# Optimization experiments

Hardware: AMD Instinct MI355X
Metric: run time of the kernel (lower is better)

The kernel has to match this reference:

```python
import jax, jax.numpy as jnp
import numpy as np

N = 100000       # nodes
E = 1600000      # edges (avg degree 16)
C_IN = 128
C_OUT = 64
C_HID = 2 * C_OUT  # 128, matches GCNEncoder's 2*out_channels hidden width


def setup_inputs() -> dict:
    key = jax.random.key(0)
    k1, k2, k3, k4 = jax.random.split(key, 4)
    x = jax.random.normal(k1, (N, C_IN), dtype=jnp.float32)
    edge_index = jax.random.randint(k2, (2, E), 0, N, dtype=jnp.int64)
    # Glorot-ish scale for the linear weights (PyG GCNConv uses glorot init)
    W1 = jax.random.normal(k3, (C_IN, C_HID), dtype=jnp.float32) / np.sqrt(C_IN)
    b1 = jnp.zeros((C_HID,), dtype=jnp.float32)
    W2 = jax.random.normal(k4, (C_HID, C_OUT), dtype=jnp.float32) / np.sqrt(C_HID)
    b2 = jnp.zeros((C_OUT,), dtype=jnp.float32)
    return {"x": x, "edge_index": edge_index, "W1": W1, "b1": b1, "W2": W2, "b2": b2}


def _gcn_conv(x, src, dst, norm_e, self_norm, W, b):
    # GCNConv: out = D^{-1/2} (A + I) D^{-1/2} (x @ W) + b
    h = x @ W                                   # [N, C'] transform first (cheaper)
    msg = h[src] * norm_e[:, None]              # [E, C'] gather + edge normalization
    agg = jax.ops.segment_sum(msg, dst, num_segments=N)  # scatter-add over targets
    return agg + self_norm[:, None] * h + b     # self-loop term + bias


def reference(x, edge_index, W1, b1, W2, b2):
    src, dst = edge_index[0], edge_index[1]
    # degrees on A + I (self-loops added), identical for both layers
    deg = jax.ops.segment_sum(jnp.ones((E,), jnp.float32), dst, num_segments=N) + 1.0
    dinv = jax.lax.rsqrt(deg)                   # deg >= 1, no zero-guard needed
    norm_e = dinv[src] * dinv[dst]              # [E]
    self_norm = dinv * dinv                     # [N]

    h = _gcn_conv(x, src, dst, norm_e, self_norm, W1, b1)
    h = jax.nn.relu(h)
    return _gcn_conv(h, src, dst, norm_e, self_norm, W2, b2)
```

## Files before the change

kernel.cpp:

```cpp
#include <hip/hip_runtime.h>
#include <hip/hip_fp16.h>

#define NN   100000
#define NE   1600000
#define CIN  128
#define CHID 128
#define COUT 64

#define NPB  256
#define NB   391
#define NBLK 128
#define CHUNK ((NE + NBLK - 1) / NBLK)
#define BPAD 2048

typedef _Float16 f16x8 __attribute__((ext_vector_type(8)));
typedef float    f32x4 __attribute__((ext_vector_type(4)));

#define NTILE 782
#define GGRID 512

__global__ void k_zrow(__half* __restrict__ g1, __half* __restrict__ g2) {
  int t = threadIdx.x;
  if (t < 128) g1[(size_t)NN * CHID + t] = __float2half(0.f);
  if (t < 64)  g2[(size_t)NN * COUT + t] = __float2half(0.f);
}

__global__ __launch_bounds__(512) void k_passA(const int* __restrict__ dst,
                                               int* __restrict__ tab) {
  __shared__ int hist[NB];
  int tid = threadIdx.x;
  for (int t = tid; t < NB; t += 512) hist[t] = 0;
  __syncthreads();
  int i0 = blockIdx.x * CHUNK;
  int i1 = min(i0 + CHUNK, NE);
  for (int i = i0 + tid; i < i1; i += 512)
    atomicAdd(&hist[((unsigned)dst[i]) >> 8], 1);
  __syncthreads();
  for (int t = tid; t < NB; t += 512)
    tab[t * NBLK + blockIdx.x] = hist[t];
}

__global__ __launch_bounds__(512) void k_bscan(const int* __restrict__ tab,
                                               int* __restrict__ bb) {
  __shared__ int s[512];
  int t = threadIdx.x;
  int v = 0;
  if (t < NB) {
    const int* row = tab + t * NBLK;
#pragma unroll 8
    for (int k = 0; k < NBLK; k++) v += row[k];
  }
  s[t] = v;
  __syncthreads();
  for (int off = 1; off < 512; off <<= 1) {
    int u = (t >= off) ? s[t - off] : 0;
    __syncthreads();
    s[t] += u;
    __syncthreads();
  }
  if (t < NB) bb[t] = s[t] - v;
  if (t == 0) bb[NB] = NE;
}

__global__ __launch_bounds__(128) void k_tabscan(int* __restrict__ tab,
                                                 const int* __restrict__ bb) {
  __shared__ int s[128];
  int b = blockIdx.x, t = threadIdx.x;
  int v = tab[b * NBLK + t];
  s[t] = v;
  __syncthreads();
  for (int off = 1; off < 128; off <<= 1) {
    int u = (t >= off) ? s[t - off] : 0;
    __syncthreads();
    s[t] += u;
    __syncthreads();
  }
  tab[b * NBLK + t] = bb[b] + s[t] - v;
}

__global__ __launch_bounds__(512) void k_passB(const int* __restrict__ src,
                                               const int* __restrict__ dst,
                                               const int* __restrict__ tab,
                                               int* __restrict__ barr) {
  __shared__ int cur[NB];
  int tid = threadIdx.x;
  for (int t = tid; t < NB; t += 512) cur[t] = tab[t * NBLK + blockIdx.x];
  __syncthreads();
  int i0 = blockIdx.x * CHUNK;
  int i1 = min(i0 + CHUNK, NE);
  for (int i = i0 + tid; i < i1; i += 512) {
    int d = dst[i];
    unsigned b = ((unsigned)d) >> 8;
    int p = atomicAdd(&cur[b], 1);
    barr[p] = (src[i] << 8) | (d & 255);
  }
}

__global__ __launch_bounds__(256) void k_l2(const int* __restrict__ barr,
                                            const int* __restrict__ bb,
                                            int* __restrict__ csr,
                                            int* __restrict__ rs,
                                            int* __restrict__ re,
                                            float* __restrict__ dinv) {
  __shared__ int lcnt[NPB];
  __shared__ int lcur[NPB];
  int b = blockIdx.x, t = threadIdx.x;
  int e0 = bb[b], e1 = bb[b + 1];
  lcnt[t] = 0;
  __syncthreads();
  for (int i = e0 + t; i < e1; i += 256) atomicAdd(&lcnt[barr[i] & 255], 1);
  __syncthreads();
  int v = lcnt[t];
  int pv = (v + 7) & ~7;
  lcur[t] = pv;
  __syncthreads();
  for (int off = 1; off < 256; off <<= 1) {
    int u = (t >= off) ? lcur[t - off] : 0;
    __syncthreads();
    lcur[t] += u;
    __syncthreads();
  }
  int pex = lcur[t] - pv;
  int start = e0 + b * BPAD + pex;
  int g = b * NPB + t;
  if (g < NN) {
    rs[g] = start;
    re[g] = start + pv;
    dinv[g] = rsqrtf((float)v + 1.0f);
  }
  __syncthreads();
  lcur[t] = start;
  for (int k = v; k < pv; k++) csr[start + k] = NN;
  __syncthreads();
  for (int i = e0 + t; i < e1; i += 256) {
    int w = barr[i];
    int p = atomicAdd(&lcur[w & 255], 1);
    csr[p] = ((unsigned)w) >> 8;
  }
}

__global__ __launch_bounds__(256, 2) void k_gemm1(const float* __restrict__ X,
                                                  const float* __restrict__ W,
                                                  const float* __restrict__ dinv,
                                                  __half* __restrict__ G) {
  __shared__ _Float16 Wt[128][128];
  int tid = threadIdx.x;
  for (int i = tid; i < 128 * 32; i += 256) {
    int k = i >> 5, c4 = (i & 31) << 2;
    float4 v = ((const float4*)W)[i];
    Wt[c4 + 0][k] = (_Float16)v.x;
    Wt[c4 + 1][k] = (_Float16)v.y;
    Wt[c4 + 2][k] = (_Float16)v.z;
    Wt[c4 + 3][k] = (_Float16)v.w;
  }
  __syncthreads();
  int wv = tid >> 6, lane = tid & 63;
  int l15 = lane & 15, g = lane >> 4;

  f16x8 wf[8][4];
#pragma unroll
  for (int cf = 0; cf < 8; cf++)
#pragma unroll
    for (int ks = 0; ks < 4; ks++)
      wf[cf][ks] = *(const f16x8*)&Wt[cf * 16 + l15][ks * 32 + g * 8];

  for (int t = blockIdx.x; t < NTILE; t += GGRID) {
    int rowbase = t * 128 + wv * 32;
    f32x4 acc[2][8];
#pragma unroll
    for (int i = 0; i < 2; i++)
#pragma unroll
      for (int j = 0; j < 8; j++) acc[i][j] = (f32x4){0.f, 0.f, 0.f, 0.f};

    int r0 = min(rowbase + l15, NN - 1);
    int r1 = min(rowbase + 16 + l15, NN - 1);
    const float* p0 = X + (size_t)r0 * CIN + g * 8;
    const float* p1 = X + (size_t)r1 * CIN + g * 8;

    float4 u0a = *(const float4*)p0, u0b = *(const float4*)(p0 + 4);
    float4 u1a = *(const float4*)p1, u1b = *(const float4*)(p1 + 4);

#pragma unroll
    for (int ks = 0; ks < 4; ks++) {
      f16x8 xa, xb;
      xa[0] = (_Float16)u0a.x; xa[1] = (_Float16)u0a.y;
      xa[2] = (_Float16)u0a.z; xa[3] = (_Float16)u0a.w;
      xa[4] = (_Float16)u0b.x; xa[5] = (_Float16)u0b.y;
      xa[6] = (_Float16)u0b.z; xa[7] = (_Float16)u0b.w;
      xb[0] = (_Float16)u1a.x; xb[1] = (_Float16)u1a.y;
      xb[2] = (_Float16)u1a.z; xb[3] = (_Float16)u1a.w;
      xb[4] = (_Float16)u1b.x; xb[5] = (_Float16)u1b.y;
      xb[6] = (_Float16)u1b.z; xb[7] = (_Float16)u1b.w;
      if (ks < 3) {
        int o = (ks + 1) * 32;
        u0a = *(const float4*)(p0 + o); u0b = *(const float4*)(p0 + o + 4);
        u1a = *(const float4*)(p1 + o); u1b = *(const float4*)(p1 + o + 4);
      }
#pragma unroll
      for (int cf = 0; cf < 8; cf++) {
        acc[0][cf] = __builtin_amdgcn_mfma_f32_16x16x32_f16(wf[cf][ks], xa, acc[0][cf], 0, 0, 0);
        acc[1][cf] = __builtin_amdgcn_mfma_f32_16x16x32_f16(wf[cf][ks], xb, acc[1][cf], 0, 0, 0);
      }
    }

#pragma unroll
    for (int rf = 0; rf < 2; rf++) {
      int row = rowbase + rf * 16 + l15;
      if (row < NN) {
        float dn = dinv[row];
#pragma unroll
        for (int cf = 0; cf < 8; cf++) {
          int col = cf * 16 + g * 4;
          __half2 h0 = __half2(__float2half(dn * acc[rf][cf][0]),
                               __float2half(dn * acc[rf][cf][1]));
          __half2 h1 = __half2(__float2half(dn * acc[rf][cf][2]),
                               __float2half(dn * acc[rf][cf][3]));
          uint2 s;
          s.x = *(unsigned*)&h0;
          s.y = *(unsigned*)&h1;
          *(uint2*)(G + (size_t)row * CHID + col) = s;
        }
      }
    }
  }
}

__global__ __launch_bounds__(256, 2) void k_gemm2(const __half* __restrict__ X,
                                                  const float* __restrict__ W,
                                                  const float* __restrict__ dinv,
                                                  __half* __restrict__ G) {
  __shared__ _Float16 Wt[64][128];
  int tid = threadIdx.x;
  for (int i = tid; i < 128 * 16; i += 256) {
    int k = i >> 4, c4 = (i & 15) << 2;
    float4 v = ((const float4*)W)[i];
    Wt[c4 + 0][k] = (_Float16)v.x;
    Wt[c4 + 1][k] = (_Float16)v.y;
    Wt[c4 + 2][k] = (_Float16)v.z;
    Wt[c4 + 3][k] = (_Float16)v.w;
  }
  __syncthreads();
  int wv = tid >> 6, lane = tid & 63;
  int l15 = lane & 15, g = lane >> 4;

  f16x8 wf[4][4];
#pragma unroll
  for (int cf = 0; cf < 4; cf++)
#pragma unroll
    for (int ks = 0; ks < 4; ks++)
      wf[cf][ks] = *(const f16x8*)&Wt[cf * 16 + l15][ks * 32 + g * 8];

  for (int t = blockIdx.x; t < NTILE; t += GGRID) {
    int rowbase = t * 128 + wv * 32;
    f32x4 acc[2][4];
#pragma unroll
    for (int i = 0; i < 2; i++)
#pragma unroll
      for (int j = 0; j < 4; j++) acc[i][j] = (f32x4){0.f, 0.f, 0.f, 0.f};

    int r0 = min(rowbase + l15, NN - 1);
    int r1 = min(rowbase + 16 + l15, NN - 1);
    const _Float16* p0 = (const _Float16*)X + (size_t)r0 * CHID + g * 8;
    const _Float16* p1 = (const _Float16*)X + (size_t)r1 * CHID + g * 8;

    f16x8 xa = *(const f16x8*)p0;
    f16x8 xb = *(const f16x8*)p1;

#pragma unroll
    for (int ks = 0; ks < 4; ks++) {
      f16x8 ca = xa, cb = xb;
      if (ks < 3) {
        int o = (ks + 1) * 32;
        xa = *(const f16x8*)(p0 + o);
        xb = *(const f16x8*)(p1 + o);
      }
#pragma unroll
      for (int cf = 0; cf < 4; cf++) {
        acc[0][cf] = __builtin_amdgcn_mfma_f32_16x16x32_f16(wf[cf][ks], ca, acc[0][cf], 0, 0, 0);
        acc[1][cf] = __builtin_amdgcn_mfma_f32_16x16x32_f16(wf[cf][ks], cb, acc[1][cf], 0, 0, 0);
      }
    }

#pragma unroll
    for (int rf = 0; rf < 2; rf++) {
      int row = rowbase + rf * 16 + l15;
      if (row < NN) {
        float dn = dinv[row];
#pragma unroll
        for (int cf = 0; cf < 4; cf++) {
          int col = cf * 16 + g * 4;
          __half2 h0 = __half2(__float2half(dn * acc[rf][cf][0]),
                               __float2half(dn * acc[rf][cf][1]));
          __half2 h1 = __half2(__float2half(dn * acc[rf][cf][2]),
                               __float2half(dn * acc[rf][cf][3]));
          uint2 s;
          s.x = *(unsigned*)&h0;
          s.y = *(unsigned*)&h1;
          *(uint2*)(G + (size_t)row * COUT + col) = s;
        }
      }
    }
  }
}

#define ACC8(A, V)                                                  \
  {                                                                 \
    float2 f;                                                       \
    f = __half22float2(*(__half2*)&(V).x); A[0] += f.x; A[1] += f.y; \
    f = __half22float2(*(__half2*)&(V).y); A[2] += f.x; A[3] += f.y; \
    f = __half22float2(*(__half2*)&(V).z); A[4] += f.x; A[5] += f.y; \
    f = __half22float2(*(__half2*)&(V).w); A[6] += f.x; A[7] += f.y; \
  }

__global__ __launch_bounds__(256) void k_agg1(const __half* __restrict__ g,
                                              const int* __restrict__ rs,
                                              const int* __restrict__ re,
                                              const float* __restrict__ dinv,
                                              const int* __restrict__ csr,
                                              const float* __restrict__ b,
                                              __half* __restrict__ o) {
  int wid = (blockIdx.x * blockDim.x + threadIdx.x) >> 6;
  int lane = threadIdx.x & 63;
  if (wid >= NN) return;
  int q = lane >> 4, ql = lane & 15;
  const uint4* gp = (const uint4*)g;

  float aA[8] = {0.f, 0.f, 0.f, 0.f, 0.f, 0.f, 0.f, 0.f};
  float aB[8] = {0.f, 0.f, 0.f, 0.f, 0.f, 0.f, 0.f, 0.f};

  if (q == 0) {
    uint4 v = gp[(size_t)wid * 16 + ql];
    ACC8(aA, v);
  }

  int i0 = rs[wid], i1 = re[wid];
  for (int i = i0; i < i1; i += 8) {
    int sA = csr[i + q];
    int sB = csr[i + 4 + q];
    uint4 vA = gp[(size_t)sA * 16 + ql];
    uint4 vB = gp[(size_t)sB * 16 + ql];
    ACC8(aA, vA);
    ACC8(aB, vB);
  }

  float r[8];
#pragma unroll
  for (int c = 0; c < 8; c++) {
    float t = aA[c] + aB[c];
    t += __shfl_xor(t, 16);
    t += __shfl_xor(t, 32);
    r[c] = t;
  }
  if (q == 0) {
    float dn = dinv[wid];
    float4 b0 = *(const float4*)(b + 8 * ql);
    float4 b1 = *(const float4*)(b + 8 * ql + 4);
    __half2 h[4];
    h[0] = __half2(__float2half(fmaxf(fmaf(dn, r[0], b0.x), 0.f)),
                   __float2half(fmaxf(fmaf(dn, r[1], b0.y), 0.f)));
    h[1] = __half2(__float2half(fmaxf(fmaf(dn, r[2], b0.z), 0.f)),
                   __float2half(fmaxf(fmaf(dn, r[3], b0.w), 0.f)));
    h[2] = __half2(__float2half(fmaxf(fmaf(dn, r[4], b1.x), 0.f)),
                   __float2half(fmaxf(fmaf(dn, r[5], b1.y), 0.f)));
    h[3] = __half2(__float2half(fmaxf(fmaf(dn, r[6], b1.z), 0.f)),
                   __float2half(fmaxf(fmaf(dn, r[7], b1.w), 0.f)));
    *(uint4*)(o + (size_t)wid * CHID + 8 * ql) = *(uint4*)h;
  }
}

__global__ __launch_bounds__(256) void k_agg2(const __half* __restrict__ g,
                                              const int* __restrict__ rs,
                                              const int* __restrict__ re,
                                              const float* __restrict__ dinv,
                                              const int* __restrict__ csr,
                                              const float* __restrict__ b,
                                              float* __restrict__ o) {
  int wid = (blockIdx.x * blockDim.x + threadIdx.x) >> 6;
  int lane = threadIdx.x & 63;
  if (wid >= NN) return;
  int g8 = lane >> 3, gl = lane & 7;
  const uint4* gp = (const uint4*)g;

  float aA[8] = {0.f, 0.f, 0.f, 0.f, 0.f, 0.f, 0.f, 0.f};

  if (g8 == 0) {
    uint4 v = gp[(size_t)wid * 8 + gl];
    ACC8(aA, v);
  }

  int i0 = rs[wid], i1 = re[wid];
  for (int i = i0; i < i1; i += 8) {
    int s = csr[i + g8];
    uint4 v = gp[(size_t)s * 8 + gl];
    ACC8(aA, v);
  }

  float r[8];
#pragma unroll
  for (int c = 0; c < 8; c++) {
    float t = aA[c];
    t += __shfl_xor(t, 8);
    t += __shfl_xor(t, 16);
    t += __shfl_xor(t, 32);
    r[c] = t;
  }
  if (g8 == 0) {
    float dn = dinv[wid];
    float4 b0 = *(const float4*)(b + 8 * gl);
    float4 b1 = *(const float4*)(b + 8 * gl + 4);
    float4 o0 = make_float4(fmaf(dn, r[0], b0.x), fmaf(dn, r[1], b0.y),
                            fmaf(dn, r[2], b0.z), fmaf(dn, r[3], b0.w));
    float4 o1v = make_float4(fmaf(dn, r[4], b1.x), fmaf(dn, r[5], b1.y),
                             fmaf(dn, r[6], b1.z), fmaf(dn, r[7], b1.w));
    *(float4*)(o + (size_t)wid * COUT + 8 * gl) = o0;
    *(float4*)(o + (size_t)wid * COUT + 8 * gl + 4) = o1v;
  }
}


extern "C" void kernel_launch(void* const* d_in, const int* in_sizes, int n_in,
                              void* d_out, int out_size, void* d_ws, size_t ws_size,
                              hipStream_t stream) {
  const float* x  = (const float*)d_in[0];
  const int*   ei = (const int*)d_in[1];
  const float* W1 = (const float*)d_in[2];
  const float* b1 = (const float*)d_in[3];
  const float* W2 = (const float*)d_in[4];
  const float* b2 = (const float*)d_in[5];
  float* out = (float*)d_out;

  const int* esrc = ei;
  const int* edst = ei + NE;

  char* p = (char*)d_ws;
  __half* g1 = (__half*)p;    p += (size_t)(NN + 1) * CHID * 2;
  __half* o1 = (__half*)p;    p += (size_t)NN * CHID * 2;
  __half* g2 = (__half*)p;    p += (size_t)(NN + 1) * COUT * 2;
  int* rs  = (int*)p;         p += (size_t)NN * 4;
  int* re  = (int*)p;         p += (size_t)NN * 4;
  float* dinv = (float*)p;    p += (size_t)NN * 4;
  int* tab = (int*)p;         p += (size_t)NB * NBLK * 4;
  int* bb  = (int*)p;         p += (size_t)(NB + 1) * 4;
  int* barr = (int*)p;        p += (size_t)NE * 4;
  int* csr = (int*)p;         p += (size_t)(NE + NB * BPAD) * 4;

  hipLaunchKernelGGL(k_zrow, dim3(1), dim3(128), 0, stream, g1, g2);

  hipLaunchKernelGGL(k_passA, dim3(NBLK), dim3(512), 0, stream, edst, tab);
  hipLaunchKernelGGL(k_bscan, dim3(1), dim3(512), 0, stream, tab, bb);
  hipLaunchKernelGGL(k_tabscan, dim3(NB), dim3(128), 0, stream, tab, bb);
  hipLaunchKernelGGL(k_passB, dim3(NBLK), dim3(512), 0, stream, esrc, edst, tab, barr);
  hipLaunchKernelGGL(k_l2, dim3(NB), dim3(256), 0, stream, barr, bb, csr, rs, re, dinv);

  hipLaunchKernelGGL(k_gemm1, dim3(GGRID), dim3(256), 0, stream, x, W1, dinv, g1);
  hipLaunchKernelGGL(k_agg1, dim3((NN + 3) / 4), dim3(256), 0, stream, g1, rs, re, dinv, csr, b1, o1);

  hipLaunchKernelGGL(k_gemm2, dim3(GGRID), dim3(256), 0, stream, o1, W2, dinv, g2);
  hipLaunchKernelGGL(k_agg2, dim3((NN + 3) / 4), dim3(256), 0, stream, g2, rs, re, dinv, csr, b2, out);
}
```

Before: 224.3 us.

## Merge scan kernels, fold zero-row init into k_l2, unroll aggregation gathers

Merges the block-base scan and per-table scan into a single one-block kernel that walks each table row serially with int4 accesses. Moves the zero-padding-row initialization into k_l2 so one kernel launch disappears. Unrolls the neighbor-gather loops in both aggregation kernels to 16 edges per iteration with extra accumulators, so more independent loads are in flight per wave. Risks: the serial row scan in one block may be slower than the previous 391-block parallel scan, and the extra accumulators raise register pressure.

Measured after the change: 227.1 us. Within noise of the previous version (+1.3%).

```diff
diff --git a/kernel.cpp b/kernel.cpp
--- a/kernel.cpp
+++ b/kernel.cpp
@@ -19,12 +19,6 @@
 #define NTILE 782
 #define GGRID 512
 
-__global__ void k_zrow(__half* __restrict__ g1, __half* __restrict__ g2) {
-  int t = threadIdx.x;
-  if (t < 128) g1[(size_t)NN * CHID + t] = __float2half(0.f);
-  if (t < 64)  g2[(size_t)NN * COUT + t] = __float2half(0.f);
-}
-
 __global__ __launch_bounds__(512) void k_passA(const int* __restrict__ dst,
                                                int* __restrict__ tab) {
   __shared__ int hist[NB];
@@ -40,8 +34,8 @@
     tab[t * NBLK + blockIdx.x] = hist[t];
 }
 
-__global__ __launch_bounds__(512) void k_bscan(const int* __restrict__ tab,
-                                               int* __restrict__ bb) {
+__global__ __launch_bounds__(512) void k_scan(int* __restrict__ tab,
+                                              int* __restrict__ bb) {
   __shared__ int s[512];
   int t = threadIdx.x;
   int v = 0;
@@ -58,24 +52,22 @@
     s[t] += u;
     __syncthreads();
   }
-  if (t < NB) bb[t] = s[t] - v;
+  int base = s[t] - v;
+  if (t < NB) bb[t] = base;
   if (t == 0) bb[NB] = NE;
-}
-
-__global__ __launch_bounds__(128) void k_tabscan(int* __restrict__ tab,
-                                                 const int* __restrict__ bb) {
-  __shared__ int s[128];
-  int b = blockIdx.x, t = threadIdx.x;
-  int v = tab[b * NBLK + t];
-  s[t] = v;
-  __syncthreads();
-  for (int off = 1; off < 128; off <<= 1) {
-    int u = (t >= off) ? s[t - off] : 0;
-    __syncthreads();
-    s[t] += u;
-    __syncthreads();
-  }
-  tab[b * NBLK + t] = bb[b] + s[t] - v;
+  if (t < NB) {
+    int run = base;
+    int* row = tab + t * NBLK;
+    for (int k = 0; k < NBLK; k += 4) {
+      int4 c = *(int4*)(row + k);
+      int4 w;
+      w.x = run; run += c.x;
+      w.y = run; run += c.y;
+      w.z = run; run += c.z;
+      w.w = run; run += c.w;
+      *(int4*)(row + k) = w;
+    }
+  }
 }
 
 __global__ __launch_bounds__(512) void k_passB(const int* __restrict__ src,
@@ -101,10 +93,16 @@
                                             int* __restrict__ csr,
                                             int* __restrict__ rs,
                                             int* __restrict__ re,
-                                            float* __restrict__ dinv) {
+                                            float* __restrict__ dinv,
+                                            __half* __restrict__ g1,
+                                            __half* __restrict__ g2) {
   __shared__ int lcnt[NPB];
   __shared__ int lcur[NPB];
   int b = blockIdx.x, t = threadIdx.x;
+  if (b == 0) {
+    if (t < 128) g1[(size_t)NN * CHID + t] = __float2half(0.f);
+    if (t < 64)  g2[(size_t)NN * COUT + t] = __float2half(0.f);
+  }
   int e0 = bb[b], e1 = bb[b + 1];
   lcnt[t] = 0;
   __syncthreads();
@@ -327,6 +325,8 @@
 
   float aA[8] = {0.f, 0.f, 0.f, 0.f, 0.f, 0.f, 0.f, 0.f};
   float aB[8] = {0.f, 0.f, 0.f, 0.f, 0.f, 0.f, 0.f, 0.f};
+  float aC[8] = {0.f, 0.f, 0.f, 0.f, 0.f, 0.f, 0.f, 0.f};
+  float aD[8] = {0.f, 0.f, 0.f, 0.f, 0.f, 0.f, 0.f, 0.f};
 
   if (q == 0) {
     uint4 v = gp[(size_t)wid * 16 + ql];
@@ -334,19 +334,30 @@
   }
 
   int i0 = rs[wid], i1 = re[wid];
-  for (int i = i0; i < i1; i += 8) {
+  int i = i0;
+  for (; i + 16 <= i1; i += 16) {
+    int sA = csr[i + q];
+    int sB = csr[i + 4 + q];
+    int sC = csr[i + 8 + q];
+    int sD = csr[i + 12 + q];
+    uint4 vA = gp[(size_t)sA * 16 + ql];
+    uint4 vB = gp[(size_t)sB * 16 + ql];
+    uint4 vC = gp[(size_t)sC * 16 + ql];
+    uint4 vD = gp[(size_t)sD * 16 + ql];
+    ACC8(aA, vA); ACC8(aB, vB); ACC8(aC, vC); ACC8(aD, vD);
+  }
+  if (i < i1) {
     int sA = csr[i + q];
     int sB = csr[i + 4 + q];
     uint4 vA = gp[(size_t)sA * 16 + ql];
     uint4 vB = gp[(size_t)sB * 16 + ql];
-    ACC8(aA, vA);
-    ACC8(aB, vB);
+    ACC8(aA, vA); ACC8(aB, vB);
   }
 
   float r[8];
 #pragma unroll
   for (int c = 0; c < 8; c++) {
-    float t = aA[c] + aB[c];
+    float t = (aA[c] + aB[c]) + (aC[c] + aD[c]);
     t += __shfl_xor(t, 16);
     t += __shfl_xor(t, 32);
     r[c] = t;
@@ -382,6 +393,7 @@
   const uint4* gp = (const uint4*)g;
 
   float aA[8] = {0.f, 0.f, 0.f, 0.f, 0.f, 0.f, 0.f, 0.f};
+  float aB[8] = {0.f, 0.f, 0.f, 0.f, 0.f, 0.f, 0.f, 0.f};
 
   if (g8 == 0) {
     uint4 v = gp[(size_t)wid * 8 + gl];
@@ -389,7 +401,15 @@
   }
 
   int i0 = rs[wid], i1 = re[wid];
-  for (int i = i0; i < i1; i += 8) {
+  int i = i0;
+  for (; i + 16 <= i1; i += 16) {
+    int sA = csr[i + g8];
+    int sB = csr[i + 8 + g8];
+    uint4 vA = gp[(size_t)sA * 8 + gl];
+    uint4 vB = gp[(size_t)sB * 8 + gl];
+    ACC8(aA, vA); ACC8(aB, vB);
+  }
+  if (i < i1) {
     int s = csr[i + g8];
     uint4 v = gp[(size_t)s * 8 + gl];
     ACC8(aA, v);
@@ -398,7 +418,7 @@
   float r[8];
 #pragma unroll
   for (int c = 0; c < 8; c++) {
-    float t = aA[c];
+    float t = aA[c] + aB[c];
     t += __shfl_xor(t, 8);
     t += __shfl_xor(t, 16);
     t += __shfl_xor(t, 32);
@@ -444,17 +464,17 @@
   int* barr = (int*)p;        p += (size_t)NE * 4;
   int* csr = (int*)p;         p += (size_t)(NE + NB * BPAD) * 4;
 
-  hipLaunchKernelGGL(k_zrow, dim3(1), dim3(128), 0, stream, g1, g2);
-
   hipLaunchKernelGGL(k_passA, dim3(NBLK), dim3(512), 0, stream, edst, tab);
-  hipLaunchKernelGGL(k_bscan, dim3(1), dim3(512), 0, stream, tab, bb);
-  hipLaunchKernelGGL(k_tabscan, dim3(NB), dim3(128), 0, stream, tab, bb);
+  hipLaunchKernelGGL(k_scan, dim3(1), dim3(512), 0, stream, tab, bb);
   hipLaunchKernelGGL(k_passB, dim3(NBLK), dim3(512), 0, stream, esrc, edst, tab, barr);
-  hipLaunchKernelGGL(k_l2, dim3(NB), dim3(256), 0, stream, barr, bb, csr, rs, re, dinv);
+  hipLaunchKernelGGL(k_l2, dim3(NB), dim3(256), 0, stream, barr, bb, csr, rs, re,
+                     dinv, g1, g2);
 
   hipLaunchKernelGGL(k_gemm1, dim3(GGRID), dim3(256), 0, stream, x, W1, dinv, g1);
-  hipLaunchKernelGGL(k_agg1, dim3((NN + 3) / 4), dim3(256), 0, stream, g1, rs, re, dinv, csr, b1, o1);
+  hipLaunchKernelGGL(k_agg1, dim3((NN + 3) / 4), dim3(256), 0, stream,
+                     g1, rs, re, dinv, csr, b1, o1);
 
   hipLaunchKernelGGL(k_gemm2, dim3(GGRID), dim3(256), 0, stream, o1, W2, dinv, g2);
-  hipLaunchKernelGGL(k_agg2, dim3((NN + 3) / 4), dim3(256), 0, stream, g2, rs, re, dinv, csr, b2, out);
-}
+  hipLaunchKernelGGL(k_agg2, dim3((NN + 3) / 4), dim3(256), 0, stream,
+                     g2, rs, re, dinv, csr, b2, out);
+}
```
